# Kernel tuning notes

Measured on AMD Instinct MI355X. Metric: run time of the kernel, lower is better.

Reference implementation:

```python
import jax, jax.numpy as jnp
import numpy as np

D_MODEL = 768
NUM_HEADS = 12
HEAD_DIM = D_MODEL // NUM_HEADS
D_FF = 3072
LN_EPS = 1e-5


def _xavier(key, shape):
    # nn.init.xavier_uniform_ on a [out, in] Linear weight
    fan_out, fan_in = shape[-2], shape[-1]
    limit = float(np.sqrt(6.0 / (fan_in + fan_out)))
    return jax.random.uniform(key, shape, jnp.float32, -limit, limit)


def setup_inputs() -> dict:
    key = jax.random.key(0)
    ks = jax.random.split(key, 10)
    x = jax.random.normal(ks[0], (4, 2048, D_MODEL), jnp.float32)
    # per-head projections stacked: [H, head_dim, d_model] (torch Linear weight layout [out, in])
    Wq = _xavier(ks[1], (NUM_HEADS, HEAD_DIM, D_MODEL))
    Wk = _xavier(ks[2], (NUM_HEADS, HEAD_DIM, D_MODEL))
    Wv = _xavier(ks[3], (NUM_HEADS, HEAD_DIM, D_MODEL))
    Wo = _xavier(ks[4], (D_MODEL, D_MODEL))
    W1 = jax.random.normal(ks[5], (D_FF, D_MODEL), jnp.float32) * 0.02
    b1 = jnp.zeros((D_FF,), jnp.float32)
    W2 = jax.random.normal(ks[6], (D_MODEL, D_FF), jnp.float32) * 0.02
    b2 = jnp.zeros((D_MODEL,), jnp.float32)
    g1 = jnp.ones((D_MODEL,), jnp.float32)
    be1 = jnp.zeros((D_MODEL,), jnp.float32)
    g2 = jnp.ones((D_MODEL,), jnp.float32)
    be2 = jnp.zeros((D_MODEL,), jnp.float32)
    return {"x": x, "Wq": Wq, "Wk": Wk, "Wv": Wv, "Wo": Wo,
            "W1": W1, "b1": b1, "W2": W2, "b2": b2,
            "g1": g1, "be1": be1, "g2": g2, "be2": be2}


def _layernorm(x, g, b):
    mu = jnp.mean(x, axis=-1, keepdims=True)
    var = jnp.mean(jnp.square(x - mu), axis=-1, keepdims=True)
    return (x - mu) * jax.lax.rsqrt(var + LN_EPS) * g + b


def reference(x, Wq, Wk, Wv, Wo, W1, b1, W2, b2, g1, be1, g2, be2):
    B, S, D = x.shape
    # all heads batched (same math as the per-head Python loop + concat)
    q = jnp.einsum('bsd,hed->bhse', x, Wq)   # [B,H,S,e]
    k = jnp.einsum('bsd,hed->bhse', x, Wk)
    v = jnp.einsum('bsd,hed->bhse', x, Wv)
    scores = jnp.einsum('bhse,bhte->bhst', q, k) / jnp.sqrt(jnp.float32(HEAD_DIM))
    attn = jax.nn.softmax(scores, axis=-1)
    ctx = jnp.einsum('bhst,bhte->bhse', attn, v)
    # concat heads along feature dim (head order matches stacking order)
    concat = ctx.transpose(0, 2, 1, 3).reshape(B, S, D)
    attn_out = concat @ Wo.T
    h = _layernorm(x + attn_out, g1, be1)
    ffn = jax.nn.relu(h @ W1.T + b1) @ W2.T + b2
    out = _layernorm(h + ffn, g2, be2)
    return out
```

## Files before the change

### kernel.cpp

```cpp
#include <hip/hip_runtime.h>

typedef unsigned short u16;
typedef unsigned int u32;
typedef __attribute__((ext_vector_type(8))) short short8;
typedef __attribute__((ext_vector_type(4))) float f32x4;
typedef __attribute__((ext_vector_type(4))) unsigned short u16x4;

__device__ __forceinline__ float b2f(u16 u){
  union { float f; unsigned int i; } c; c.i = ((unsigned int)u) << 16; return c.f;
}
__device__ __forceinline__ u16 f2b(float f){
  union { float f; unsigned int i; } c; c.f = f;
  unsigned int i = c.i;
  unsigned int r = (i + 0x7FFFu + ((i >> 16) & 1u)) >> 16;
  return (u16)r;
}

#define EXP2(x) exp2f(x)

#define GLD16(gp, lp) __builtin_amdgcn_global_load_lds( \
    (const __attribute__((address_space(1))) void*)(gp), \
    (__attribute__((address_space(3))) void*)(lp), 16, 0, 0)

__device__ __forceinline__ u32 pkbf(float lo, float hi){
  u32 r;
  asm volatile("v_cvt_pk_bf16_f32 %0, %1, %2" : "=v"(r) : "v"(lo), "v"(hi));
  return r;
}

__global__ __launch_bounds__(256) void cvt_all(
    const float* __restrict__ s0, const float* __restrict__ s1,
    const float* __restrict__ s2, const float* __restrict__ s3,
    const float* __restrict__ s4, const float* __restrict__ s5,
    const float* __restrict__ s6, u16* __restrict__ dst)
{
  const int i = (blockIdx.x * 256 + threadIdx.x) * 4;
  const float* sp;
  if      (i <  6291456) sp = s0 + i;
  else if (i <  6881280) sp = s1 + (i - 6291456);
  else if (i <  7471104) sp = s2 + (i - 6881280);
  else if (i <  8060928) sp = s3 + (i - 7471104);
  else if (i <  8650752) sp = s4 + (i - 8060928);
  else if (i < 11010048) sp = s5 + (i - 8650752);
  else                   sp = s6 + (i - 11010048);
  float4 f = *(const float4*)sp;
  u16x4 o = { f2b(f.x), f2b(f.y), f2b(f.z), f2b(f.w) };
  *(u16x4*)(dst + i) = o;
}

__global__ __launch_bounds__(256) void transpose_v(const u16* __restrict__ v,
                                                   u16* __restrict__ vt){
  __shared__ short t[64][72];
  const int plane = blockIdx.y;
  const u16* vp = v + (size_t)plane * 2048 * 64;
  u16* vtp = vt + (size_t)plane * 2048 * 64;
  const int s0 = blockIdx.x * 64;
#pragma unroll
  for (int j = 0; j < 2; j++){
    int ch = threadIdx.x + 256*j;
    int r = ch >> 3, c = (ch & 7) << 3;
    short8 val = *(const short8*)(vp + (size_t)(s0 + r)*64 + c);
#pragma unroll
    for (int jj = 0; jj < 8; jj++) t[c + jj][r] = val[jj];
  }
  __syncthreads();
#pragma unroll
  for (int j = 0; j < 2; j++){
    int ch = threadIdx.x + 256*j;
    int r = ch >> 3, c = (ch & 7) << 3;
    *(short8*)(vtp + (size_t)r*2048 + s0 + c) = *(const short8*)&t[r][c];
  }
}

enum { EPI_QKV = 0, EPI_WO = 1, EPI_FFN1 = 2, EPI_FFN2 = 3 };
__device__ __forceinline__ float KSCALE_C(){ return 0.125f * 1.44269504088896340736f; }

template<int EPI>
__global__ __launch_bounds__(256) void gemm_bt(
    const u16* __restrict__ A, const u16* __restrict__ Bm,
    int K, int gx,
    u16* __restrict__ outB,
    const float* __restrict__ auxF,
    const u16* __restrict__ auxB)
{
  __shared__ __align__(16) short Asm[128][32];
  __shared__ __align__(16) short Bsm[128][32];
  const int tid  = threadIdx.x;
  const int lane = tid & 63;
  const int wid  = tid >> 6;
  const int wr = wid >> 1, wc = wid & 1;
  const int fr = lane & 15, fq = lane >> 4;

  const int nwg = gridDim.x;
  const int lin = blockIdx.x;
  const int wg  = (lin & 7) * (nwg >> 3) + (lin >> 3);
  const int bx = wg % gx, by = wg / gx;
  const int m0 = by * 128, n0 = bx * 128;

  f32x4 acc[4][4];
#pragma unroll
  for (int i = 0; i < 4; i++)
#pragma unroll
    for (int j = 0; j < 4; j++) acc[i][j] = (f32x4){0.f, 0.f, 0.f, 0.f};

  const int lrow = lane >> 2;
  const int lcol = (lane & 3) << 3;

  for (int k0 = 0; k0 < K; k0 += 32) {
    const u16* ga = A  + (size_t)(m0 + wid*32 + lrow) * K + k0 + lcol;
    const u16* gb = Bm + (size_t)(n0 + wid*32 + lrow) * K + k0 + lcol;
    GLD16(ga,                 &Asm[wid*32][0]);
    GLD16(ga + (size_t)16*K,  &Asm[wid*32 + 16][0]);
    GLD16(gb,                 &Bsm[wid*32][0]);
    GLD16(gb + (size_t)16*K,  &Bsm[wid*32 + 16][0]);
    __syncthreads();

    short8 a[4], b[4];
#pragma unroll
    for (int i = 0; i < 4; i++) a[i] = *(const short8*)&Asm[wr*64 + i*16 + fr][fq*8];
#pragma unroll
    for (int j = 0; j < 4; j++) b[j] = *(const short8*)&Bsm[wc*64 + j*16 + fr][fq*8];
    __builtin_amdgcn_s_setprio(1);
#pragma unroll
    for (int i = 0; i < 4; i++)
#pragma unroll
      for (int j = 0; j < 4; j++)
        acc[i][j] = __builtin_amdgcn_mfma_f32_16x16x32_bf16(a[i], b[j], acc[i][j], 0, 0, 0);
    __builtin_amdgcn_s_setprio(0);
    __syncthreads();
  }

#pragma unroll
  for (int i = 0; i < 4; i++) {
    const int row0 = m0 + wr*64 + i*16 + fq*4;
#pragma unroll
    for (int j = 0; j < 4; j++) {
      const int col = n0 + wc*64 + j*16 + fr;
#pragma unroll
      for (int r = 0; r < 4; r++) {
        const int row = row0 + r;
        float val = acc[i][j][r];
        if (EPI == EPI_FFN1) {
          float o = val + auxF[col];
          o = o > 0.f ? o : 0.f;
          outB[(size_t)row * 3072 + col] = f2b(o);
        }
      }
    }
  }
}

template<int EPI>
__global__ __launch_bounds__(256) void gemm_bt64(
    const u16* __restrict__ A, const u16* __restrict__ Bm,
    int K, int gx,
    u16* __restrict__ outB,
    const float* __restrict__ auxF,
    const u16* __restrict__ auxB)
{
  __shared__ __align__(16) short Asm[64][32];
  __shared__ __align__(16) short Bsm[128][32];
  const int tid  = threadIdx.x;
  const int lane = tid & 63;
  const int wid  = tid >> 6;
  const int wr = wid >> 1, wc = wid & 1;
  const int fr = lane & 15, fq = lane >> 4;

  const int nwg = gridDim.x;
  const int lin = blockIdx.x;
  const int wg  = (lin & 7) * (nwg >> 3) + (lin >> 3);
  const int bx = wg % gx, by = wg / gx;
  const int m0 = by * 64, n0 = bx * 128;

  f32x4 acc[2][4];
#pragma unroll
  for (int i = 0; i < 2; i++)
#pragma unroll
    for (int j = 0; j < 4; j++) acc[i][j] = (f32x4){0.f, 0.f, 0.f, 0.f};

  const int lrow = lane >> 2;
  const int lcol = (lane & 3) << 3;

  for (int k0 = 0; k0 < K; k0 += 32) {
    const u16* ga = A  + (size_t)(m0 + wid*16 + lrow) * K + k0 + lcol;
    const u16* gb = Bm + (size_t)(n0 + wid*32 + lrow) * K + k0 + lcol;
    GLD16(ga,                 &Asm[wid*16][0]);
    GLD16(gb,                 &Bsm[wid*32][0]);
    GLD16(gb + (size_t)16*K,  &Bsm[wid*32 + 16][0]);
    __syncthreads();

    short8 a[2], b[4];
#pragma unroll
    for (int i = 0; i < 2; i++) a[i] = *(const short8*)&Asm[wr*32 + i*16 + fr][fq*8];
#pragma unroll
    for (int j = 0; j < 4; j++) b[j] = *(const short8*)&Bsm[wc*64 + j*16 + fr][fq*8];
    __builtin_amdgcn_s_setprio(1);
#pragma unroll
    for (int i = 0; i < 2; i++)
#pragma unroll
      for (int j = 0; j < 4; j++)
        acc[i][j] = __builtin_amdgcn_mfma_f32_16x16x32_bf16(a[i], b[j], acc[i][j], 0, 0, 0);
    __builtin_amdgcn_s_setprio(0);
    __syncthreads();
  }

#pragma unroll
  for (int i = 0; i < 2; i++) {
    const int row0 = m0 + wr*32 + i*16 + fq*4;
#pragma unroll
    for (int j = 0; j < 4; j++) {
      const int col = n0 + wc*64 + j*16 + fr;
#pragma unroll
      for (int r = 0; r < 4; r++) {
        const int row = row0 + r;
        float val = acc[i][j][r];
        if (EPI == EPI_QKV) {
          int tt = (col >= 1536) ? 2 : (col >= 768 ? 1 : 0);
          int rem = col - tt * 768;
          int h = rem >> 6, e = rem & 63;
          int bb = row >> 11, s = row & 2047;
          size_t idx = (((size_t)(tt*48 + bb*12 + h)) * 2048 + s) * 64 + e;
          if (tt == 1) val *= KSCALE_C();
          outB[idx] = f2b(val);
        } else if (EPI == EPI_WO) {
          size_t idx = (size_t)row * 768 + col;
          outB[idx] = f2b(val + b2f(auxB[idx]));
        } else {
          size_t idx = (size_t)row * 768 + col;
          outB[idx] = f2b(val + auxF[col] + b2f(auxB[idx]));
        }
      }
    }
  }
}

__global__ __launch_bounds__(512) void flash_attn(
    const u16* __restrict__ q, const u16* __restrict__ kmat, const u16* __restrict__ vtmat,
    u16* __restrict__ ctx)
{
  const int tid = threadIdx.x;
  const int lane = tid & 63, wid = tid >> 6;
  const int fr = lane & 15, fq = lane >> 4;
  const int orig = blockIdx.x;
  const int wg = (orig & 7) * 96 + (orig >> 3);
  const int qb = wg & 15;
  const int ph = wg >> 4;
  const size_t plane = (size_t)ph * 2048 * 64;
  const u16* qp  = q + plane;
  const u16* kp  = kmat + plane;
  const u16* vtp = vtmat + plane;

  __shared__ __align__(16) short Ksm[2][64][64];
  __shared__ __align__(16) short Vsm[2][64][64];

  const int qr0 = qb*128 + wid*16;
  const short8 aq0 = *(const short8*)(qp + (size_t)(qr0 + fr)*64 + fq*8);
  const short8 aq1 = *(const short8*)(qp + (size_t)(qr0 + fr)*64 + 32 + fq*8);

  short8 vones;
#pragma unroll
  for (int j = 0; j < 8; j++) vones[j] = (short)0x3F80;

  const int rA = wid*8 + (lane >> 3);
  const int cA = (((lane & 7) ^ ((rA & 3) | (((rA >> 3) & 1) << 2)))) * 8;

#define STAGE(B, KT) do { \
    GLD16(kp  + (size_t)((KT)*64 + rA)*64 + cA,  &Ksm[B][wid*8][0]); \
    GLD16(vtp + (size_t)rA*2048 + (KT)*64 + cA,  &Vsm[B][wid*8][0]); \
  } while(0)

  f32x4 o[4];
#pragma unroll
  for (int eb = 0; eb < 4; eb++) o[eb] = (f32x4){0.f, 0.f, 0.f, 0.f};
  float m = -1e30f, l = 0.f;
  const f32x4 zero = (f32x4){0.f, 0.f, 0.f, 0.f};

  STAGE(0, 0);
  __syncthreads();

  const int fK  = (fr & 3) | (((fr >> 2) & 1) << 2);
  const int kc0 = ((fq    ) ^ fK) * 8;
  const int kc1 = ((4 + fq) ^ fK) * 8;
  const int krow = (fr & 3) + 8 * (fr >> 2);
  const int fV  = (fr & 3) | (((fr >> 3) & 1) << 2);
  const int vc0 = ((fq    ) ^ fV) * 8;
  const int vc1 = ((4 + fq) ^ fV) * 8;

  int buf = 0;
  for (int kt = 0; kt < 32; ++kt) {
    if (kt < 31) STAGE(buf ^ 1, kt + 1);

    f32x4 st[2][2];
    __builtin_amdgcn_s_setprio(1);
#pragma unroll
    for (int h = 0; h < 2; h++)
#pragma unroll
      for (int c = 0; c < 2; c++) {
        const short* kr = &Ksm[buf][32*h + 4*c + krow][0];
        short8 kf0 = *(const short8*)(kr + kc0);
        short8 kf1 = *(const short8*)(kr + kc1);
        f32x4 a = __builtin_amdgcn_mfma_f32_16x16x32_bf16(kf0, aq0, zero, 0, 0, 0);
        st[h][c]  = __builtin_amdgcn_mfma_f32_16x16x32_bf16(kf1, aq1, a,    0, 0, 0);
      }
    __builtin_amdgcn_s_setprio(0);

    float t0 = fmaxf(fmaxf(st[0][0][0], st[0][0][1]), st[0][0][2]);
    float t1 = fmaxf(fmaxf(st[0][0][3], st[0][1][0]), st[0][1][1]);
    float t2 = fmaxf(fmaxf(st[0][1][2], st[0][1][3]), st[1][0][0]);
    float t3 = fmaxf(fmaxf(st[1][0][1], st[1][0][2]), st[1][0][3]);
    float t4 = fmaxf(fmaxf(st[1][1][0], st[1][1][1]), st[1][1][2]);
    float u0 = fmaxf(fmaxf(t0, t1), st[1][1][3]);
    float u1 = fmaxf(fmaxf(t2, t3), t4);
    float lm = fmaxf(u0, u1);
    lm = fmaxf(lm, __shfl_xor(lm, 16));
    lm = fmaxf(lm, __shfl_xor(lm, 32));

    if (!__all(lm <= m + 8.f)) {
      float nm = fmaxf(m, lm);
      float corr = EXP2(m - nm);
      m = nm;
      l *= corr;
#pragma unroll
      for (int eb = 0; eb < 4; eb++)
#pragma unroll
        for (int r = 0; r < 4; r++) o[eb][r] *= corr;
    }

    float p[2][2][4];
#pragma unroll
    for (int h = 0; h < 2; h++)
#pragma unroll
      for (int c = 0; c < 2; c++)
#pragma unroll
        for (int r = 0; r < 4; r++)
          p[h][c][r] = EXP2(st[h][c][r] - m);

    union { u32 u[4]; short8 s8; } pf0, pf1;
    pf0.u[0] = pkbf(p[0][0][0], p[0][0][1]);
    pf0.u[1] = pkbf(p[0][0][2], p[0][0][3]);
    pf0.u[2] = pkbf(p[0][1][0], p[0][1][1]);
    pf0.u[3] = pkbf(p[0][1][2], p[0][1][3]);
    pf1.u[0] = pkbf(p[1][0][0], p[1][0][1]);
    pf1.u[1] = pkbf(p[1][0][2], p[1][0][3]);
    pf1.u[2] = pkbf(p[1][1][0], p[1][1][1]);
    pf1.u[3] = pkbf(p[1][1][2], p[1][1][3]);

    __builtin_amdgcn_s_setprio(1);
    f32x4 ol = __builtin_amdgcn_mfma_f32_16x16x32_bf16(vones, pf0.s8, zero, 0, 0, 0);
    ol       = __builtin_amdgcn_mfma_f32_16x16x32_bf16(vones, pf1.s8, ol,   0, 0, 0);
#pragma unroll
    for (int eb = 0; eb < 4; eb++) {
      const short* vr = &Vsm[buf][eb*16 + fr][0];
      o[eb] = __builtin_amdgcn_mfma_f32_16x16x32_bf16(*(const short8*)(vr + vc0), pf0.s8, o[eb], 0, 0, 0);
      o[eb] = __builtin_amdgcn_mfma_f32_16x16x32_bf16(*(const short8*)(vr + vc1), pf1.s8, o[eb], 0, 0, 0);
    }
    __builtin_amdgcn_s_setprio(0);
    l += ol[0];

    __syncthreads();
    buf ^= 1;
  }
#undef STAGE

  const float inv = 1.0f / l;
  const int s = qr0 + fr;
  u16* cp = ctx + ((size_t)((ph/12)*2048 + s)) * 768 + (ph%12)*64;
#pragma unroll
  for (int eb = 0; eb < 4; eb++) {
    u16x4 w = { f2b(o[eb][0]*inv), f2b(o[eb][1]*inv), f2b(o[eb][2]*inv), f2b(o[eb][3]*inv) };
    *(u16x4*)(cp + eb*16 + fq*4) = w;
  }
}

template<int F32OUT>
__global__ __launch_bounds__(256) void ln_k(const u16* __restrict__ in,
    const float* __restrict__ g, const float* __restrict__ be, void* __restrict__ outp)
{
  const int lane = threadIdx.x & 63, wid = threadIdx.x >> 6;
  const int row = blockIdx.x * 4 + wid;
  const u16* p = in + (size_t)row * 768;
  float v[12];
  float s = 0.f, s2 = 0.f;
#pragma unroll
  for (int i = 0; i < 6; i++) {
    ushort2 uv = *(const ushort2*)(p + i*128 + lane*2);
    v[2*i]   = b2f(uv.x);
    v[2*i+1] = b2f(uv.y);
    s += v[2*i] + v[2*i+1];
    s2 += v[2*i]*v[2*i] + v[2*i+1]*v[2*i+1];
  }
#pragma unroll
  for (int msk = 1; msk < 64; msk <<= 1) { s += __shfl_xor(s, msk); s2 += __shfl_xor(s2, msk); }
  const float mu = s * (1.f/768.f);
  const float var = s2 * (1.f/768.f) - mu*mu;
  const float rstd = rsqrtf(var + 1e-5f);
#pragma unroll
  for (int i = 0; i < 6; i++) {
    int c = i*128 + lane*2;
    float o0 = (v[2*i]   - mu) * rstd * g[c]   + be[c];
    float o1 = (v[2*i+1] - mu) * rstd * g[c+1] + be[c+1];
    if (F32OUT) {
      float2 w = { o0, o1 };
      *(float2*)((float*)outp + (size_t)row*768 + c) = w;
    } else {
      ushort2 w = { f2b(o0), f2b(o1) };
      *(ushort2*)((u16*)outp + (size_t)row*768 + c) = w;
    }
  }
}

extern "C" void kernel_launch(void* const* d_in, const int* in_sizes, int n_in,
                              void* d_out, int out_size, void* d_ws, size_t ws_size,
                              hipStream_t stream)
{
  const float* x   = (const float*)d_in[0];
  const float* Wq  = (const float*)d_in[1];
  const float* Wk  = (const float*)d_in[2];
  const float* Wv  = (const float*)d_in[3];
  const float* Wo  = (const float*)d_in[4];
  const float* W1  = (const float*)d_in[5];
  const float* b1  = (const float*)d_in[6];
  const float* W2  = (const float*)d_in[7];
  const float* b2  = (const float*)d_in[8];
  const float* g1  = (const float*)d_in[9];
  const float* be1 = (const float*)d_in[10];
  const float* g2  = (const float*)d_in[11];
  const float* be2 = (const float*)d_in[12];
  float* out = (float*)d_out;

  char* ws = (char*)d_ws;
  u16* xb     = (u16*)(ws + 0);
  u16* Wqkv_b = (u16*)(ws + 12582912);
  u16* Wo_b   = (u16*)(ws + 16121856);
  u16* W1_b   = (u16*)(ws + 17301504);
  u16* W2_b   = (u16*)(ws + 22020096);
  u16* qkv    = (u16*)(ws + 26738688);
  u16* ctxb   = (u16*)(ws + 64487424);
  u16* hidden = (u16*)(ws + 26738688);
  u16* vt     = (u16*)(ws + 77070336);
  u16* resid1 = (u16*)(ws + 77070336);
  u16* hb     = (u16*)(ws + 102236160);
  u16* pre2   = (u16*)(ws + 77070336);

  cvt_all<<<dim3(13056), 256, 0, stream>>>(x, Wq, Wk, Wv, Wo, W1, W2, (u16*)ws);

  gemm_bt64<EPI_QKV><<<dim3(2304), 256, 0, stream>>>(
      xb, Wqkv_b, 768, 18, qkv, nullptr, nullptr);

  u16* qb_ = qkv;
  u16* kb_ = qkv + 6291456;
  u16* vb_ = qkv + 12582912;

  transpose_v<<<dim3(32, 48), 256, 0, stream>>>(vb_, vt);

  flash_attn<<<dim3(768), 512, 0, stream>>>(qb_, kb_, vt, ctxb);

  gemm_bt64<EPI_WO><<<dim3(768), 256, 0, stream>>>(
      ctxb, Wo_b, 768, 6, resid1, nullptr, xb);

  ln_k<0><<<2048, 256, 0, stream>>>(resid1, g1, be1, hb);

  gemm_bt<EPI_FFN1><<<dim3(1536), 256, 0, stream>>>(
      hb, W1_b, 768, 24, hidden, b1, nullptr);

  gemm_bt64<EPI_FFN2><<<dim3(768), 256, 0, stream>>>(
      hidden, W2_b, 3072, 6, pre2, b2, hb);

  ln_k<1><<<2048, 256, 0, stream>>>(pre2, g2, be2, out);
}
```

Measured before the change: 323.2 us.

## Use split-K 128x128 GEMMs for Wo/FFN2 and fuse residual adds into LayerNorm

Replaces the 64x128-tile GEMMs for the Wo and FFN2 projections with a 128x128-tile split-K kernel. It writes two bf16 partial sums, and a new LayerNorm kernel adds those partials, the residual and the bias before normalising. The QKV projection moves to the 128x128 tile kernel with half the blocks, and the softmax exp2 switches to the native hardware exp2. The aim is better data reuse per tile while keeping enough workgroups in flight. The cost is extra partial-sum traffic, plus extra bf16 rounding from storing each partial separately.

```diff
diff --git a/kernel.cpp b/kernel.cpp
--- a/kernel.cpp
+++ b/kernel.cpp
@@ -6,6 +6,9 @@
 typedef __attribute__((ext_vector_type(4))) float f32x4;
 typedef __attribute__((ext_vector_type(4))) unsigned short u16x4;
 
+extern "C" __device__ float __ocml_native_exp2_f32(float);
+#define EXP2(x) __ocml_native_exp2_f32(x)
+
 __device__ __forceinline__ float b2f(u16 u){
   union { float f; unsigned int i; } c; c.i = ((unsigned int)u) << 16; return c.f;
 }
@@ -15,8 +18,6 @@
   unsigned int r = (i + 0x7FFFu + ((i >> 16) & 1u)) >> 16;
   return (u16)r;
 }
-
-#define EXP2(x) exp2f(x)
 
 #define GLD16(gp, lp) __builtin_amdgcn_global_load_lds( \
     (const __attribute__((address_space(1))) void*)(gp), \
@@ -72,7 +73,7 @@
   }
 }
 
-enum { EPI_QKV = 0, EPI_WO = 1, EPI_FFN1 = 2, EPI_FFN2 = 3 };
+enum { EPI_QKV = 0, EPI_FFN1 = 2 };
 __device__ __forceinline__ float KSCALE_C(){ return 0.125f * 1.44269504088896340736f; }
 
 template<int EPI>
@@ -80,8 +81,7 @@
     const u16* __restrict__ A, const u16* __restrict__ Bm,
     int K, int gx,
     u16* __restrict__ outB,
-    const float* __restrict__ auxF,
-    const u16* __restrict__ auxB)
+    const float* __restrict__ auxF)
 {
   __shared__ __align__(16) short Asm[128][32];
   __shared__ __align__(16) short Bsm[128][32];
@@ -133,80 +133,6 @@
 #pragma unroll
   for (int i = 0; i < 4; i++) {
     const int row0 = m0 + wr*64 + i*16 + fq*4;
-#pragma unroll
-    for (int j = 0; j < 4; j++) {
-      const int col = n0 + wc*64 + j*16 + fr;
-#pragma unroll
-      for (int r = 0; r < 4; r++) {
-        const int row = row0 + r;
-        float val = acc[i][j][r];
-        if (EPI == EPI_FFN1) {
-          float o = val + auxF[col];
-          o = o > 0.f ? o : 0.f;
-          outB[(size_t)row * 3072 + col] = f2b(o);
-        }
-      }
-    }
-  }
-}
-
-template<int EPI>
-__global__ __launch_bounds__(256) void gemm_bt64(
-    const u16* __restrict__ A, const u16* __restrict__ Bm,
-    int K, int gx,
-    u16* __restrict__ outB,
-    const float* __restrict__ auxF,
-    const u16* __restrict__ auxB)
-{
-  __shared__ __align__(16) short Asm[64][32];
-  __shared__ __align__(16) short Bsm[128][32];
-  const int tid  = threadIdx.x;
-  const int lane = tid & 63;
-  const int wid  = tid >> 6;
-  const int wr = wid >> 1, wc = wid & 1;
-  const int fr = lane & 15, fq = lane >> 4;
-
-  const int nwg = gridDim.x;
-  const int lin = blockIdx.x;
-  const int wg  = (lin & 7) * (nwg >> 3) + (lin >> 3);
-  const int bx = wg % gx, by = wg / gx;
-  const int m0 = by * 64, n0 = bx * 128;
-
-  f32x4 acc[2][4];
-#pragma unroll
-  for (int i = 0; i < 2; i++)
-#pragma unroll
-    for (int j = 0; j < 4; j++) acc[i][j] = (f32x4){0.f, 0.f, 0.f, 0.f};
-
-  const int lrow = lane >> 2;
-  const int lcol = (lane & 3) << 3;
-
-  for (int k0 = 0; k0 < K; k0 += 32) {
-    const u16* ga = A  + (size_t)(m0 + wid*16 + lrow) * K + k0 + lcol;
-    const u16* gb = Bm + (size_t)(n0 + wid*32 + lrow) * K + k0 + lcol;
-    GLD16(ga,                 &Asm[wid*16][0]);
-    GLD16(gb,                 &Bsm[wid*32][0]);
-    GLD16(gb + (size_t)16*K,  &Bsm[wid*32 + 16][0]);
-    __syncthreads();
-
-    short8 a[2], b[4];
-#pragma unroll
-    for (int i = 0; i < 2; i++) a[i] = *(const short8*)&Asm[wr*32 + i*16 + fr][fq*8];
-#pragma unroll
-    for (int j = 0; j < 4; j++) b[j] = *(const short8*)&Bsm[wc*64 + j*16 + fr][fq*8];
-    __builtin_amdgcn_s_setprio(1);
-#pragma unroll
-    for (int i = 0; i < 2; i++)
-#pragma unroll
-      for (int j = 0; j < 4; j++)
-        acc[i][j] = __builtin_amdgcn_mfma_f32_16x16x32_bf16(a[i], b[j], acc[i][j], 0, 0, 0);
-    __builtin_amdgcn_s_setprio(0);
-    __syncthreads();
-  }
-
-#pragma unroll
-  for (int i = 0; i < 2; i++) {
-    const int row0 = m0 + wr*32 + i*16 + fq*4;
 #pragma unroll
     for (int j = 0; j < 4; j++) {
       const int col = n0 + wc*64 + j*16 + fr;
@@ -222,14 +148,82 @@
           size_t idx = (((size_t)(tt*48 + bb*12 + h)) * 2048 + s) * 64 + e;
           if (tt == 1) val *= KSCALE_C();
           outB[idx] = f2b(val);
-        } else if (EPI == EPI_WO) {
-          size_t idx = (size_t)row * 768 + col;
-          outB[idx] = f2b(val + b2f(auxB[idx]));
         } else {
-          size_t idx = (size_t)row * 768 + col;
-          outB[idx] = f2b(val + auxF[col] + b2f(auxB[idx]));
+          float o = val + auxF[col];
+          o = o > 0.f ? o : 0.f;
+          outB[(size_t)row * 3072 + col] = f2b(o);
         }
       }
+    }
+  }
+}
+
+__global__ __launch_bounds__(256) void gemm_split(
+    const u16* __restrict__ A, const u16* __restrict__ Bm,
+    int K, int KS, int gx,
+    u16* __restrict__ outP)
+{
+  __shared__ __align__(16) short Asm[128][32];
+  __shared__ __align__(16) short Bsm[128][32];
+  const int tid  = threadIdx.x;
+  const int lane = tid & 63;
+  const int wid  = tid >> 6;
+  const int wr = wid >> 1, wc = wid & 1;
+  const int fr = lane & 15, fq = lane >> 4;
+
+  const int nwg = gridDim.x;
+  const int lin = blockIdx.x;
+  const int wg  = (lin & 7) * (nwg >> 3) + (lin >> 3);
+  const int per = gx * 64;
+  const int ks  = wg / per;
+  const int rem = wg % per;
+  const int bx = rem % gx, by = rem / gx;
+  const int m0 = by * 128, n0 = bx * 128;
+  const int kbase = ks * KS;
+
+  f32x4 acc[4][4];
+#pragma unroll
+  for (int i = 0; i < 4; i++)
+#pragma unroll
+    for (int j = 0; j < 4; j++) acc[i][j] = (f32x4){0.f, 0.f, 0.f, 0.f};
+
+  const int lrow = lane >> 2;
+  const int lcol = (lane & 3) << 3;
+
+  for (int k0 = 0; k0 < KS; k0 += 32) {
+    const u16* ga = A  + (size_t)(m0 + wid*32 + lrow) * K + kbase + k0 + lcol;
+    const u16* gb = Bm + (size_t)(n0 + wid*32 + lrow) * K + kbase + k0 + lcol;
+    GLD16(ga,                 &Asm[wid*32][0]);
+    GLD16(ga + (size_t)16*K,  &Asm[wid*32 + 16][0]);
+    GLD16(gb,                 &Bsm[wid*32][0]);
+    GLD16(gb + (size_t)16*K,  &Bsm[wid*32 + 16][0]);
+    __syncthreads();
+
+    short8 a[4], b[4];
+#pragma unroll
+    for (int i = 0; i < 4; i++) a[i] = *(const short8*)&Asm[wr*64 + i*16 + fr][fq*8];
+#pragma unroll
+    for (int j = 0; j < 4; j++) b[j] = *(const short8*)&Bsm[wc*64 + j*16 + fr][fq*8];
+    __builtin_amdgcn_s_setprio(1);
+#pragma unroll
+    for (int i = 0; i < 4; i++)
+#pragma unroll
+      for (int j = 0; j < 4; j++)
+        acc[i][j] = __builtin_amdgcn_mfma_f32_16x16x32_bf16(a[i], b[j], acc[i][j], 0, 0, 0);
+    __builtin_amdgcn_s_setprio(0);
+    __syncthreads();
+  }
+
+  u16* op = outP + (size_t)ks * 6291456;
+#pragma unroll
+  for (int i = 0; i < 4; i++) {
+    const int row0 = m0 + wr*64 + i*16 + fq*4;
+#pragma unroll
+    for (int j = 0; j < 4; j++) {
+      const int col = n0 + wc*64 + j*16 + fr;
+#pragma unroll
+      for (int r = 0; r < 4; r++)
+        op[(size_t)(row0 + r) * 768 + col] = f2b(acc[i][j][r]);
     }
   }
 }
@@ -372,22 +366,29 @@
   }
 }
 
-template<int F32OUT>
-__global__ __launch_bounds__(256) void ln_k(const u16* __restrict__ in,
+template<int HASBIAS, int F32OUT>
+__global__ __launch_bounds__(256) void ln_add_k(
+    const u16* __restrict__ p0, const u16* __restrict__ p1, const u16* __restrict__ extra,
+    const float* __restrict__ bias,
     const float* __restrict__ g, const float* __restrict__ be, void* __restrict__ outp)
 {
   const int lane = threadIdx.x & 63, wid = threadIdx.x >> 6;
   const int row = blockIdx.x * 4 + wid;
-  const u16* p = in + (size_t)row * 768;
+  const size_t base = (size_t)row * 768;
   float v[12];
   float s = 0.f, s2 = 0.f;
 #pragma unroll
   for (int i = 0; i < 6; i++) {
-    ushort2 uv = *(const ushort2*)(p + i*128 + lane*2);
-    v[2*i]   = b2f(uv.x);
-    v[2*i+1] = b2f(uv.y);
-    s += v[2*i] + v[2*i+1];
-    s2 += v[2*i]*v[2*i] + v[2*i+1]*v[2*i+1];
+    int c = i*128 + lane*2;
+    ushort2 a0 = *(const ushort2*)(p0 + base + c);
+    ushort2 a1 = *(const ushort2*)(p1 + base + c);
+    ushort2 ax = *(const ushort2*)(extra + base + c);
+    float v0 = b2f(a0.x) + b2f(a1.x) + b2f(ax.x);
+    float v1 = b2f(a0.y) + b2f(a1.y) + b2f(ax.y);
+    if (HASBIAS) { v0 += bias[c]; v1 += bias[c+1]; }
+    v[2*i] = v0; v[2*i+1] = v1;
+    s += v0 + v1;
+    s2 += v0*v0 + v1*v1;
   }
 #pragma unroll
   for (int msk = 1; msk < 64; msk <<= 1) { s += __shfl_xor(s, msk); s2 += __shfl_xor(s2, msk); }
@@ -401,10 +402,10 @@
     float o1 = (v[2*i+1] - mu) * rstd * g[c+1] + be[c+1];
     if (F32OUT) {
       float2 w = { o0, o1 };
-      *(float2*)((float*)outp + (size_t)row*768 + c) = w;
+      *(float2*)((float*)outp + base + c) = w;
     } else {
       ushort2 w = { f2b(o0), f2b(o1) };
-      *(ushort2*)((u16*)outp + (size_t)row*768 + c) = w;
+      *(ushort2*)((u16*)outp + base + c) = w;
     }
   }
 }
@@ -438,14 +439,13 @@
   u16* ctxb   = (u16*)(ws + 64487424);
   u16* hidden = (u16*)(ws + 26738688);
   u16* vt     = (u16*)(ws + 77070336);
-  u16* resid1 = (u16*)(ws + 77070336);
+  u16* part   = (u16*)(ws + 77070336);
   u16* hb     = (u16*)(ws + 102236160);
-  u16* pre2   = (u16*)(ws + 77070336);
 
   cvt_all<<<dim3(13056), 256, 0, stream>>>(x, Wq, Wk, Wv, Wo, W1, W2, (u16*)ws);
 
-  gemm_bt64<EPI_QKV><<<dim3(2304), 256, 0, stream>>>(
-      xb, Wqkv_b, 768, 18, qkv, nullptr, nullptr);
+  gemm_bt<EPI_QKV><<<dim3(1152), 256, 0, stream>>>(
+      xb, Wqkv_b, 768, 18, qkv, nullptr);
 
   u16* qb_ = qkv;
   u16* kb_ = qkv + 6291456;
@@ -455,16 +455,17 @@
 
   flash_attn<<<dim3(768), 512, 0, stream>>>(qb_, kb_, vt, ctxb);
 
-  gemm_bt64<EPI_WO><<<dim3(768), 256, 0, stream>>>(
-      ctxb, Wo_b, 768, 6, resid1, nullptr, xb);
-
-  ln_k<0><<<2048, 256, 0, stream>>>(resid1, g1, be1, hb);
+  u16* p0 = part;
+  u16* p1 = part + 6291456;
+
+  gemm_split<<<dim3(768), 256, 0, stream>>>(ctxb, Wo_b, 768, 384, 6, part);
+
+  ln_add_k<0, 0><<<2048, 256, 0, stream>>>(p0, p1, xb, nullptr, g1, be1, hb);
 
   gemm_bt<EPI_FFN1><<<dim3(1536), 256, 0, stream>>>(
-      hb, W1_b, 768, 24, hidden, b1, nullptr);
-
-  gemm_bt64<EPI_FFN2><<<dim3(768), 256, 0, stream>>>(
-      hidden, W2_b, 3072, 6, pre2, b2, hb);
-
-  ln_k<1><<<2048, 256, 0, stream>>>(pre2, g2, be2, out);
-}
+      hb, W1_b, 768, 24, hidden, b1);
+
+  gemm_split<<<dim3(768), 256, 0, stream>>>(hidden, W2_b, 3072, 1536, 6, part);
+
+  ln_add_k<1, 1><<<2048, 256, 0, stream>>>(p0, p1, hb, b2, g2, be2, out);
+}
```

Result: faster. 276.0 us (-14.6%).
